# Optimization experiments

Measured on AMD Instinct MI355X. Metric: run time of the kernel, lower is better.

## Reference

```python
import jax, jax.numpy as jnp
import numpy as np

B, L, D = 4, 2048, 1024
E, F, H = 6, 1536, 512  # experts, d_ff, router hidden
TOP_K = 2
LN_EPS = 1e-5

def setup_inputs() -> dict:
    key = jax.random.key(0)
    ks = jax.random.split(key, 8)
    s = lambda fan: 1.0 / np.sqrt(fan)
    return {
        "x": jax.random.normal(ks[0], (B, L, D), jnp.float32),
        "r1_w": jax.random.normal(ks[1], (D, H), jnp.float32) * s(D),
        "r1_b": jnp.zeros((H,), jnp.float32),
        "ln_g": jnp.ones((H,), jnp.float32),
        "ln_b": jnp.zeros((H,), jnp.float32),
        "r2_w": jax.random.normal(ks[2], (H, E), jnp.float32) * s(H),
        "r2_b": jnp.zeros((E,), jnp.float32),
        "temp": jnp.ones((1,), jnp.float32),
        "route_bias": jnp.zeros((E,), jnp.float32),
        "W1": jax.random.normal(ks[3], (E, D, F), jnp.float32) * s(D),
        "b1": jnp.zeros((E, F), jnp.float32),
        "W2": jax.random.normal(ks[4], (E, F, D), jnp.float32) * s(F),
        "b2": jnp.zeros((E, D), jnp.float32),
    }

def reference(x, r1_w, r1_b, ln_g, ln_b, r2_w, r2_b, temp, route_bias, W1, b1, W2, b2):
    b, l, d = x.shape
    xf = x.reshape(-1, d)                       # [N, D]
    n = xf.shape[0]
    # Router: Linear -> LayerNorm -> GELU(exact) -> Linear
    h = xf @ r1_w + r1_b                        # [N, H]
    mu = jnp.mean(h, axis=-1, keepdims=True)
    var = jnp.mean((h - mu) ** 2, axis=-1, keepdims=True)
    h = (h - mu) * jax.lax.rsqrt(var + LN_EPS) * ln_g + ln_b
    h = jax.nn.gelu(h, approximate=False)
    logits = (h @ r2_w + r2_b) / temp + route_bias   # [N, E]
    p = jax.nn.softmax(logits, axis=-1)
    top_v, top_i = jax.lax.top_k(p, TOP_K)      # [N, k]
    probs = jnp.zeros_like(p).at[jnp.arange(n)[:, None], top_i].set(top_v)  # [N, E]
    # Dense all-expert MLPs (faithful to source, which computes every expert)
    hh = jnp.einsum('nd,edf->enf', xf, W1) + b1[:, None, :]   # [E, N, F]
    even = (jnp.arange(W1.shape[0]) % 2 == 0)[:, None, None]
    act = jnp.where(even, jax.nn.gelu(hh, approximate=False), jax.nn.silu(hh))
    eo = jnp.einsum('enf,efd->end', act, W2) + b2[:, None, :]  # [E, N, D]
    out = jnp.einsum('ne,end->nd', probs, eo)   # weighted combine
    return out.reshape(b, l, d)
```

## Files before the change

kernel.cpp:

```cpp
#include <hip/hip_runtime.h>
#include <hip/hip_bf16.h>
#include <stdint.h>

typedef __bf16 bf16;
typedef bf16 bf16x8 __attribute__((ext_vector_type(8)));
typedef bf16 bf16x4 __attribute__((ext_vector_type(4)));
typedef float f32x4 __attribute__((ext_vector_type(4)));
typedef int i32x4 __attribute__((ext_vector_type(4)));

#define N_TOK 8192
#define D_MODEL 1024
#define H_R 512
#define N_EXP 6
#define F_FF 1536
#define FLAG_CAP 1024

__device__ __forceinline__ float erf_fast(float x) {
    float ax = fabsf(x);
    float t = 1.0f / (1.0f + 0.3275911f * ax);
    float p = t * (0.254829592f + t * (-0.284496736f + t * (1.421413741f +
              t * (-1.453152027f + t * 1.061405429f))));
    float r = 1.0f - p * __expf(-ax * ax);
    return copysignf(r, x);
}
__device__ __forceinline__ float gelu_f(float x) {
    return 0.5f * x * (1.0f + erf_fast(x * 0.70710678118654752f));
}
__device__ __forceinline__ float silu_f(float x) {
    return x * (1.0f / (1.0f + __expf(-x)));
}

typedef __attribute__((address_space(1))) const void* gas1;
typedef __attribute__((address_space(3))) void* las3;

__device__ __forceinline__ void gload16(const void* g, void* l) {
    __builtin_amdgcn_global_load_lds((gas1)g, (las3)l, 16, 0, 0);
}

__device__ __forceinline__ int swz_src_q(int c) {
    return (((c & 3) - ((c >> 2) >> 1)) & 3);
}


__global__ __launch_bounds__(256) void convert_x_split(
    const float* __restrict__ x, bf16* __restrict__ xh, bf16* __restrict__ xl) {
    size_t i = ((size_t)blockIdx.x * 256 + threadIdx.x) * 8;
    f32x4 a = *(const f32x4*)(x + i);
    f32x4 b = *(const f32x4*)(x + i + 4);
    float v[8] = {a[0], a[1], a[2], a[3], b[0], b[1], b[2], b[3]};
    bf16x8 vh, vl;
    #pragma unroll
    for (int k = 0; k < 8; ++k) {
        bf16 h = (bf16)v[k];
        vh[k] = h;
        vl[k] = (bf16)(v[k] - (float)h);
    }
    *(bf16x8*)(xh + i) = vh;
    *(bf16x8*)(xl + i) = vl;
}

__global__ __launch_bounds__(256) void transpose_bf16_64(
    const float* __restrict__ in, bf16* __restrict__ out, int R, int C) {
    __shared__ float tile[64][65];
    const float* inp = in + (size_t)blockIdx.z * R * C;
    bf16* op = out + (size_t)blockIdx.z * R * C;
    int tx = threadIdx.x & 15, ty = threadIdx.x >> 4;
    int r0 = blockIdx.y * 64, c0 = blockIdx.x * 64;
    #pragma unroll
    for (int p = 0; p < 4; ++p) {
        int row = p * 16 + ty;
        f32x4 v = *(const f32x4*)(inp + (size_t)(r0 + row) * C + c0 + tx * 4);
        tile[row][tx * 4 + 0] = v[0];
        tile[row][tx * 4 + 1] = v[1];
        tile[row][tx * 4 + 2] = v[2];
        tile[row][tx * 4 + 3] = v[3];
    }
    __syncthreads();
    #pragma unroll
    for (int p = 0; p < 4; ++p) {
        int cc = p * 16 + ty;
        bf16x4 o;
        #pragma unroll
        for (int k = 0; k < 4; ++k) o[k] = (bf16)tile[tx * 4 + k][cc];
        *(bf16x4*)(op + (size_t)(c0 + cc) * R + r0 + tx * 4) = o;
    }
}

__global__ __launch_bounds__(256) void transpose_split(
    const float* __restrict__ in, bf16* __restrict__ oh, bf16* __restrict__ ol,
    int R, int C) {
    __shared__ float tile[32][33];
    int tx = threadIdx.x & 31, ty = threadIdx.x >> 5;
    int r0 = blockIdx.y * 32, c0 = blockIdx.x * 32;
    #pragma unroll
    for (int yy = ty; yy < 32; yy += 8)
        tile[yy][tx] = in[(size_t)(r0 + yy) * C + c0 + tx];
    __syncthreads();
    #pragma unroll
    for (int yy = ty; yy < 32; yy += 8) {
        float v = tile[tx][yy];
        bf16 h = (bf16)v;
        size_t o = (size_t)(c0 + yy) * R + r0 + tx;
        oh[o] = h;
        ol[o] = (bf16)(v - (float)h);
    }
}


struct SMemStd {
    alignas(16) bf16 As[128 * 32];
    alignas(16) bf16 Bs[128 * 32];
};

__device__ __forceinline__ void gemm_core_async(
    const bf16* gA0, const bf16* gA1, const bf16* gB0, const bf16* gB1,
    int K, bf16* As, bf16* Bs, f32x4 acc[4][4]) {
    const int tid = threadIdx.x;
    const int lane = tid & 63;
    const int w = tid >> 6;
    const int wm = w & 1, wn = w >> 1;
    const int lc = lane & 15;
    const int koff = ((((lane >> 4) + (lc >> 1)) & 3) * 8);
    bf16* lA0 = As + w * 512;
    bf16* lA1 = As + 2048 + w * 512;
    bf16* lB0 = Bs + w * 512;
    bf16* lB1 = Bs + 2048 + w * 512;
    for (int kb = 0; kb < K; kb += 32) {
        __syncthreads();
        gload16(gA0 + kb, lA0);
        gload16(gA1 + kb, lA1);
        gload16(gB0 + kb, lB0);
        gload16(gB1 + kb, lB1);
        __syncthreads();
        bf16x8 af[4], bfr[4];
        #pragma unroll
        for (int i = 0; i < 4; ++i)
            af[i] = *(const bf16x8*)(As + (wm * 64 + i * 16 + lc) * 32 + koff);
        #pragma unroll
        for (int j = 0; j < 4; ++j)
            bfr[j] = *(const bf16x8*)(Bs + (wn * 64 + j * 16 + lc) * 32 + koff);
        #pragma unroll
        for (int i = 0; i < 4; ++i)
            #pragma unroll
            for (int j = 0; j < 4; ++j)
                acc[i][j] = __builtin_amdgcn_mfma_f32_16x16x32_bf16(af[i], bfr[j], acc[i][j], 0, 0, 0);
    }
}


__global__ __launch_bounds__(256) void router_gemm1_3(
    const bf16* __restrict__ xh, const bf16* __restrict__ xl,
    const bf16* __restrict__ wTh, const bf16* __restrict__ wTl,
    float* __restrict__ hp0, float* __restrict__ hp1, float* __restrict__ hp2) {
    __shared__ SMemStd sm;
    const int z = blockIdx.z;
    const bf16* Ab = (z == 2) ? xl : xh;
    const bf16* Bb = (z == 1) ? wTl : wTh;
    float* hp = (z == 0) ? hp0 : (z == 1 ? hp1 : hp2);
    const int tid = threadIdx.x;
    const int mbase = blockIdx.y * 128, nbase = blockIdx.x * 128;
    int c0 = tid, c1 = tid + 256;
    const bf16* gA0 = Ab + (size_t)(mbase + (c0 >> 2)) * D_MODEL + swz_src_q(c0) * 8;
    const bf16* gA1 = Ab + (size_t)(mbase + (c1 >> 2)) * D_MODEL + swz_src_q(c1) * 8;
    const bf16* Bt = Bb + (size_t)nbase * D_MODEL;
    const bf16* gB0 = Bt + (size_t)(c0 >> 2) * D_MODEL + swz_src_q(c0) * 8;
    const bf16* gB1 = Bt + (size_t)(c1 >> 2) * D_MODEL + swz_src_q(c1) * 8;
    f32x4 acc[4][4] = {};
    gemm_core_async(gA0, gA1, gB0, gB1, D_MODEL, sm.As, sm.Bs, acc);
    const int lane = tid & 63;
    const int w = tid >> 6;
    const int wm = w & 1, wn = w >> 1;
    const int lc = lane & 15, quad = lane >> 4;
    #pragma unroll
    for (int i = 0; i < 4; ++i)
        #pragma unroll
        for (int j = 0; j < 4; ++j) {
            int col = nbase + wn * 64 + j * 16 + lc;
            #pragma unroll
            for (int r = 0; r < 4; ++r) {
                int row = mbase + wm * 64 + i * 16 + quad * 4 + r;
                hp[(size_t)row * H_R + col] = acc[i][j][r];
            }
        }
}


__global__ __launch_bounds__(256) void ln_router2(
    const float* __restrict__ hp0, const float* __restrict__ hp1,
    const float* __restrict__ hp2, const float* __restrict__ r1b,
    const float* __restrict__ g, const float* __restrict__ bta,
    const float* __restrict__ r2w, const float* __restrict__ r2b,
    const float* __restrict__ temp, const float* __restrict__ rbias,
    int* __restrict__ top_i, float* __restrict__ top_p,
    int* __restrict__ flaglist, int* __restrict__ meta) {
    __shared__ float Wl[H_R * N_EXP];
    int tid = threadIdx.x;
    for (int i = tid; i < H_R * N_EXP; i += 256) Wl[i] = r2w[i];
    __syncthreads();
    int w = tid >> 6, lane = tid & 63;
    int t = blockIdx.x * 4 + w;
    size_t rbase = (size_t)t * H_R;
    int k0 = lane * 8;
    float v[8];
    {
        f32x4 a0 = *(const f32x4*)(hp0 + rbase + k0);
        f32x4 a1 = *(const f32x4*)(hp0 + rbase + k0 + 4);
        f32x4 b0 = *(const f32x4*)(hp1 + rbase + k0);
        f32x4 b1 = *(const f32x4*)(hp1 + rbase + k0 + 4);
        f32x4 c0 = *(const f32x4*)(hp2 + rbase + k0);
        f32x4 c1 = *(const f32x4*)(hp2 + rbase + k0 + 4);
        f32x4 d0 = *(const f32x4*)(r1b + k0);
        f32x4 d1 = *(const f32x4*)(r1b + k0 + 4);
        #pragma unroll
        for (int k = 0; k < 4; ++k) {
            v[k]     = a0[k] + b0[k] + c0[k] + d0[k];
            v[k + 4] = a1[k] + b1[k] + c1[k] + d1[k];
        }
    }
    float s = 0.f;
    #pragma unroll
    for (int k = 0; k < 8; ++k) s += v[k];
    #pragma unroll
    for (int off = 32; off; off >>= 1) s += __shfl_xor(s, off);
    float mu = s * (1.0f / H_R);
    float q = 0.f;
    #pragma unroll
    for (int k = 0; k < 8; ++k) { float d = v[k] - mu; q += d * d; }
    #pragma unroll
    for (int off = 32; off; off >>= 1) q += __shfl_xor(q, off);
    float scl = 1.0f / sqrtf(q * (1.0f / H_R) + 1e-5f);
    f32x4 g0 = *(const f32x4*)(g + k0), g1 = *(const f32x4*)(g + k0 + 4);
    f32x4 b0 = *(const f32x4*)(bta + k0), b1v = *(const f32x4*)(bta + k0 + 4);
    float G[8] = {g0[0], g0[1], g0[2], g0[3], g1[0], g1[1], g1[2], g1[3]};
    float B[8] = {b0[0], b0[1], b0[2], b0[3], b1v[0], b1v[1], b1v[2], b1v[3]};
    float acc[N_EXP] = {};
    #pragma unroll
    for (int k = 0; k < 8; ++k) {
        float y = gelu_f((v[k] - mu) * scl * G[k] + B[k]);
        const float* wr = &Wl[(k0 + k) * N_EXP];
        #pragma unroll
        for (int e = 0; e < N_EXP; ++e) acc[e] += y * wr[e];
    }
    #pragma unroll
    for (int e = 0; e < N_EXP; ++e)
        #pragma unroll
        for (int off = 32; off; off >>= 1) acc[e] += __shfl_xor(acc[e], off);
    if (lane == 0) {
        float tinv = 1.0f / temp[0];
        float lg[N_EXP];
// ... 128 lines not shown
        #pragma unroll
        for (int e = 0; e < N_EXP; ++e) S[e][tid] += tmp[e];
        __syncthreads();
    }
    if (tid == 0) {
        int o = 0;
        #pragma unroll
        for (int e = 0; e < N_EXP; ++e) {
            segbase[e] = o;
            int tot = S[e][RP_T - 1];
            meta[e] = tot;
            meta[8 + e] = o;
            o += tot;
        }
        segbase[N_EXP] = o;
    }
    __syncthreads();
    int pos[N_EXP];
    #pragma unroll
    for (int e = 0; e < N_EXP; ++e)
        pos[e] = segbase[e] + S[e][tid] - cnt[e];
    #pragma unroll
    for (int k = 0; k < 2 * RP_TOK; ++k) {
        int e = e_loc[k];
        int a = 0;
        #pragma unroll
        for (int ee = 0; ee < N_EXP; ++ee) if (e == ee) a = pos[ee]++;
        atok[a] = t0 + (k >> 1);
        ainv[2 * t0 + k] = a;
    }
}


__global__ __launch_bounds__(256) void expert_gemm1(
    const bf16* __restrict__ xb, const bf16* __restrict__ W1T,
    const float* __restrict__ b1, const int* __restrict__ meta,
    const int* __restrict__ atok, bf16* __restrict__ act) {
    int e = blockIdx.z;
    int rows = meta[e];
    int mloc = blockIdx.y * 128;
    if (mloc >= rows) return;
    int base = meta[8 + e];
    __shared__ SMemStd sm;
    int tid = threadIdx.x;
    int nbase = blockIdx.x * 128;
    int c0 = tid, c1 = tid + 256;
    int r0 = mloc + (c0 >> 2); if (r0 > rows - 1) r0 = rows - 1;
    int r1 = mloc + (c1 >> 2); if (r1 > rows - 1) r1 = rows - 1;
    const bf16* gA0 = xb + (size_t)atok[base + r0] * D_MODEL + swz_src_q(c0) * 8;
    const bf16* gA1 = xb + (size_t)atok[base + r1] * D_MODEL + swz_src_q(c1) * 8;
    const bf16* Bt = W1T + ((size_t)e * F_FF + nbase) * D_MODEL;
    const bf16* gB0 = Bt + (size_t)(c0 >> 2) * D_MODEL + swz_src_q(c0) * 8;
    const bf16* gB1 = Bt + (size_t)(c1 >> 2) * D_MODEL + swz_src_q(c1) * 8;
    f32x4 acc[4][4] = {};
    gemm_core_async(gA0, gA1, gB0, gB1, D_MODEL, sm.As, sm.Bs, acc);
    const int lane = tid & 63;
    const int w = tid >> 6;
    const int wm = w & 1, wn = w >> 1;
    const int lc = lane & 15, quad = lane >> 4;
    bool odd = (e & 1) != 0;
    #pragma unroll
    for (int i = 0; i < 4; ++i)
        #pragma unroll
        for (int j = 0; j < 4; ++j) {
            int col = nbase + wn * 64 + j * 16 + lc;
            float bias = b1[e * F_FF + col];
            #pragma unroll
            for (int r = 0; r < 4; ++r) {
                int rloc = mloc + wm * 64 + i * 16 + quad * 4 + r;
                if (rloc < rows) {
                    float vv = acc[i][j][r] + bias;
                    vv = odd ? silu_f(vv) : gelu_f(vv);
                    act[(size_t)(base + rloc) * F_FF + col] = (bf16)vv;
                }
            }
        }
}

__global__ __launch_bounds__(256) void expert_gemm2(
    const bf16* __restrict__ act, const bf16* __restrict__ W2T,
    const float* __restrict__ b2, const int* __restrict__ meta,
    float* __restrict__ eo) {
    int e = blockIdx.z;
    int rows = meta[e];
    int mloc = blockIdx.y * 128;
    if (mloc >= rows) return;
    int base = meta[8 + e];
    __shared__ SMemStd sm;
    int tid = threadIdx.x;
    int nbase = blockIdx.x * 128;
    int c0 = tid, c1 = tid + 256;
    int r0 = mloc + (c0 >> 2); if (r0 > rows - 1) r0 = rows - 1;
    int r1 = mloc + (c1 >> 2); if (r1 > rows - 1) r1 = rows - 1;
    const bf16* gA0 = act + (size_t)(base + r0) * F_FF + swz_src_q(c0) * 8;
    const bf16* gA1 = act + (size_t)(base + r1) * F_FF + swz_src_q(c1) * 8;
    const bf16* Bt = W2T + ((size_t)e * D_MODEL + nbase) * F_FF;
    const bf16* gB0 = Bt + (size_t)(c0 >> 2) * F_FF + swz_src_q(c0) * 8;
    const bf16* gB1 = Bt + (size_t)(c1 >> 2) * F_FF + swz_src_q(c1) * 8;
    f32x4 acc[4][4] = {};
    gemm_core_async(gA0, gA1, gB0, gB1, F_FF, sm.As, sm.Bs, acc);
    const int lane = tid & 63;
    const int w = tid >> 6;
    const int wm = w & 1, wn = w >> 1;
    const int lc = lane & 15, quad = lane >> 4;
    #pragma unroll
    for (int i = 0; i < 4; ++i)
        #pragma unroll
        for (int j = 0; j < 4; ++j) {
            int col = nbase + wn * 64 + j * 16 + lc;
            float bias = b2[e * D_MODEL + col];
            #pragma unroll
            for (int r = 0; r < 4; ++r) {
                int rloc = mloc + wm * 64 + i * 16 + quad * 4 + r;
                if (rloc < rows)
                    eo[(size_t)(base + rloc) * D_MODEL + col] = acc[i][j][r] + bias;
            }
        }
}


__global__ __launch_bounds__(256) void combine_kernel(
    const float* __restrict__ eo, const int* __restrict__ ainv,
    const float* __restrict__ top_p, float* __restrict__ out) {
    int t = blockIdx.x;
    int s0 = ainv[2 * t], s1 = ainv[2 * t + 1];
    float p0 = top_p[2 * t], p1 = top_p[2 * t + 1];
    int c = threadIdx.x * 4;
    f32x4 a = *(const f32x4*)(eo + (size_t)s0 * D_MODEL + c);
    f32x4 b = *(const f32x4*)(eo + (size_t)s1 * D_MODEL + c);
    f32x4 o;
    #pragma unroll
    for (int k = 0; k < 4; ++k) o[k] = a[k] * p0 + b[k] * p1;
    *(f32x4*)(out + (size_t)t * D_MODEL + c) = o;
}


extern "C" void kernel_launch(void* const* d_in, const int* in_sizes, int n_in,
                              void* d_out, int out_size, void* d_ws, size_t ws_size,
                              hipStream_t stream) {
    const float* x     = (const float*)d_in[0];
    const float* r1w   = (const float*)d_in[1];
    const float* r1b   = (const float*)d_in[2];
    const float* lng   = (const float*)d_in[3];
    const float* lnb   = (const float*)d_in[4];
    const float* r2w   = (const float*)d_in[5];
    const float* r2b   = (const float*)d_in[6];
    const float* temp  = (const float*)d_in[7];
    const float* rbias = (const float*)d_in[8];
    const float* W1    = (const float*)d_in[9];
    const float* b1    = (const float*)d_in[10];
    const float* W2    = (const float*)d_in[11];
    const float* b2    = (const float*)d_in[12];
    float* out = (float*)d_out;

    char* ws = (char*)d_ws;
    size_t off = 0;
    auto alloc = [&](size_t bytes) -> void* {
        void* p = ws + off;
        off = (off + bytes + 255) & ~(size_t)255;
        return p;
    };
    bf16*  xh    = (bf16*)alloc((size_t)N_TOK * D_MODEL * 2);
    bf16*  xl    = (bf16*)alloc((size_t)N_TOK * D_MODEL * 2);
    bf16*  r1wTh = (bf16*)alloc((size_t)H_R * D_MODEL * 2);
    bf16*  r1wTl = (bf16*)alloc((size_t)H_R * D_MODEL * 2);
    bf16*  W1T   = (bf16*)alloc((size_t)N_EXP * F_FF * D_MODEL * 2);
    bf16*  W2T   = (bf16*)alloc((size_t)N_EXP * D_MODEL * F_FF * 2);
    float* hp0   = (float*)alloc((size_t)N_TOK * H_R * 4);
    int*   top_i = (int*)alloc((size_t)N_TOK * 2 * 4);
    float* top_p = (float*)alloc((size_t)N_TOK * 2 * 4);
    int*   meta  = (int*)alloc(256);
    int*   flags = (int*)alloc(FLAG_CAP * 4);
    int*   atok  = (int*)alloc((size_t)2 * N_TOK * 4);
    int*   ainv  = (int*)alloc((size_t)2 * N_TOK * 4);
    bf16*  actb  = (bf16*)alloc((size_t)2 * N_TOK * F_FF * 2);
    float* eo    = (float*)alloc((size_t)2 * N_TOK * D_MODEL * 4);
    float* hp1 = (float*)actb;
    float* hp2 = (float*)((char*)actb + (size_t)N_TOK * H_R * 4);
    (void)ws_size; (void)n_in; (void)in_sizes;

    hipMemsetAsync(meta, 0, 256, stream);

    convert_x_split<<<(N_TOK * D_MODEL) / (256 * 8), 256, 0, stream>>>(x, xh, xl);
    transpose_split<<<dim3(H_R / 32, D_MODEL / 32, 1), 256, 0, stream>>>(
        r1w, r1wTh, r1wTl, D_MODEL, H_R);
    transpose_bf16_64<<<dim3(F_FF / 64, D_MODEL / 64, N_EXP), 256, 0, stream>>>(
        W1, W1T, D_MODEL, F_FF);
    transpose_bf16_64<<<dim3(D_MODEL / 64, F_FF / 64, N_EXP), 256, 0, stream>>>(
        W2, W2T, F_FF, D_MODEL);

    router_gemm1_3<<<dim3(H_R / 128, N_TOK / 128, 3), 256, 0, stream>>>(
        xh, xl, r1wTh, r1wTl, hp0, hp1, hp2);
    ln_router2<<<N_TOK / 4, 256, 0, stream>>>(
        hp0, hp1, hp2, r1b, lng, lnb, r2w, r2b, temp, rbias, top_i, top_p, flags, meta);
    router_rescue<<<FLAG_CAP, 256, 0, stream>>>(
        x, r1w, r1b, lng, lnb, r2w, r2b, temp, rbias, flags, meta, top_i, top_p);
    route_pack<<<1, RP_T, 0, stream>>>(top_i, meta, atok, ainv);

    expert_gemm1<<<dim3(F_FF / 128, N_TOK / 128, N_EXP), 256, 0, stream>>>(
        xh, W1T, b1, meta, atok, actb);
    expert_gemm2<<<dim3(D_MODEL / 128, N_TOK / 128, N_EXP), 256, 0, stream>>>(
        actb, W2T, b2, meta, eo);
    combine_kernel<<<N_TOK, 256, 0, stream>>>(eo, ainv, top_p, out);
}
```

Baseline: 554.8 us.

## Use 256x256 double-buffered MFMA tiles with 512 threads for expert GEMMs

Adds a new GEMM core that computes 256x256 output tiles with 8 waves, a K-step of 64, a swizzled LDS layout, and double-buffered global-to-LDS loads. Each wave works through its 128x64 sub-tile in four phases, interleaving fragment loads with MFMA bursts under barriers and s_setprio. Both expert GEMMs switch to this core with 128KB of dynamic shared memory. The larger tiles raise data reuse and cut LDS traffic per FLOP. In exchange, fewer blocks are launched, there is more padded work on partial row tiles, and LDS use allows only one block per CU.

```diff
diff --git a/kernel.cpp b/kernel.cpp
--- a/kernel.cpp
+++ b/kernel.cpp
@@ -144,6 +144,131 @@
             #pragma unroll
             for (int j = 0; j < 4; ++j)
                 acc[i][j] = __builtin_amdgcn_mfma_f32_16x16x32_bf16(af[i], bfr[j], acc[i][j], 0, 0, 0);
+    }
+}
+
+
+__device__ __forceinline__ void gemm256_core(
+    const bf16* a0, const bf16* a1, const bf16* a2, const bf16* a3,
+    const bf16* b0, const bf16* b1, const bf16* b2, const bf16* b3,
+    int K, bf16* As, bf16* Bs, f32x4 acc[8][4])
+{
+    const int tid = threadIdx.x;
+    const int w = tid >> 6;
+    const int lane = tid & 63;
+    const int lc = lane & 15, qdv = lane >> 4;
+    const int wm = w & 1, wn = w >> 1;
+    const int wst = w * 512;
+    const int NT = K >> 6;
+    gload16(a0, As + wst);
+    gload16(a1, As + 4096 + wst);
+    gload16(a2, As + 8192 + wst);
+    gload16(a3, As + 12288 + wst);
+    gload16(b0, Bs + wst);
+    gload16(b1, Bs + 4096 + wst);
+    gload16(b2, Bs + 8192 + wst);
+    gload16(b3, Bs + 12288 + wst);
+    a0 += 64; a1 += 64; a2 += 64; a3 += 64;
+    b0 += 64; b1 += 64; b2 += 64; b3 += 64;
+    __syncthreads();
+    const int rA0 = wm * 128 + lc;
+    const int rB0 = wn * 64 + lc;
+    int bo = 0;
+    for (int t = 0; t < NT; ++t) {
+        const int nb = bo ^ 16384;
+        bf16x8 af[4][2], bfr[2][2];
+        if (t + 1 < NT) {
+            gload16(a0, As + nb + wst);
+            gload16(a1, As + nb + 4096 + wst);
+            gload16(a2, As + nb + 8192 + wst);
+            gload16(a3, As + nb + 12288 + wst);
+            gload16(b0, Bs + nb + wst);
+            gload16(b1, Bs + nb + 4096 + wst);
+            gload16(b2, Bs + nb + 8192 + wst);
+            gload16(b3, Bs + nb + 12288 + wst);
+            a0 += 64; a1 += 64; a2 += 64; a3 += 64;
+            b0 += 64; b1 += 64; b2 += 64; b3 += 64;
+        }
+        #pragma unroll
+        for (int i = 0; i < 4; ++i) {
+            int row = rA0 + i * 16;
+            #pragma unroll
+            for (int s = 0; s < 2; ++s)
+                af[i][s] = *(const bf16x8*)(As + bo + row * 64 + (((s * 4 + qdv) + row) & 7) * 8);
+        }
+        #pragma unroll
+        for (int j = 0; j < 2; ++j) {
+            int row = rB0 + j * 16;
+            #pragma unroll
+            for (int s = 0; s < 2; ++s)
+                bfr[j][s] = *(const bf16x8*)(Bs + bo + row * 64 + (((s * 4 + qdv) + row) & 7) * 8);
+        }
+        __builtin_amdgcn_s_barrier();
+        __builtin_amdgcn_s_setprio(1);
+        #pragma unroll
+        for (int i = 0; i < 4; ++i)
+            #pragma unroll
+            for (int j = 0; j < 2; ++j)
+                #pragma unroll
+                for (int s = 0; s < 2; ++s)
+                    acc[i][j] = __builtin_amdgcn_mfma_f32_16x16x32_bf16(af[i][s], bfr[j][s], acc[i][j], 0, 0, 0);
+        __builtin_amdgcn_s_setprio(0);
+        __builtin_amdgcn_s_barrier();
+        #pragma unroll
+        for (int j = 0; j < 2; ++j) {
+            int row = rB0 + 32 + j * 16;
+            #pragma unroll
+            for (int s = 0; s < 2; ++s)
+                bfr[j][s] = *(const bf16x8*)(Bs + bo + row * 64 + (((s * 4 + qdv) + row) & 7) * 8);
+        }
+        __builtin_amdgcn_s_barrier();
+        __builtin_amdgcn_s_setprio(1);
+        #pragma unroll
+        for (int i = 0; i < 4; ++i)
+            #pragma unroll
+            for (int j = 0; j < 2; ++j)
+                #pragma unroll
+                for (int s = 0; s < 2; ++s)
+                    acc[i][2 + j] = __builtin_amdgcn_mfma_f32_16x16x32_bf16(af[i][s], bfr[j][s], acc[i][2 + j], 0, 0, 0);
+        __builtin_amdgcn_s_setprio(0);
+        __builtin_amdgcn_s_barrier();
+        #pragma unroll
+        for (int i = 0; i < 4; ++i) {
+            int row = rA0 + 64 + i * 16;
+            #pragma unroll
+            for (int s = 0; s < 2; ++s)
+                af[i][s] = *(const bf16x8*)(As + bo + row * 64 + (((s * 4 + qdv) + row) & 7) * 8);
+        }
+        __builtin_amdgcn_s_barrier();
+        __builtin_amdgcn_s_setprio(1);
+        #pragma unroll
+        for (int i = 0; i < 4; ++i)
+            #pragma unroll
+            for (int j = 0; j < 2; ++j)
+                #pragma unroll
+                for (int s = 0; s < 2; ++s)
+                    acc[4 + i][2 + j] = __builtin_amdgcn_mfma_f32_16x16x32_bf16(af[i][s], bfr[j][s], acc[4 + i][2 + j], 0, 0, 0);
+        __builtin_amdgcn_s_setprio(0);
+        __builtin_amdgcn_s_barrier();
+        #pragma unroll
+        for (int j = 0; j < 2; ++j) {
+            int row = rB0 + j * 16;
+            #pragma unroll
+            for (int s = 0; s < 2; ++s)
+                bfr[j][s] = *(const bf16x8*)(Bs + bo + row * 64 + (((s * 4 + qdv) + row) & 7) * 8);
+        }
+        __builtin_amdgcn_s_barrier();
+        __builtin_amdgcn_s_setprio(1);
+        #pragma unroll
+        for (int i = 0; i < 4; ++i)
+            #pragma unroll
+            for (int j = 0; j < 2; ++j)
+                #pragma unroll
+                for (int s = 0; s < 2; ++s)
+                    acc[4 + i][j] = __builtin_amdgcn_mfma_f32_16x16x32_bf16(af[i][s], bfr[j][s], acc[4 + i][j], 0, 0, 0);
+        __builtin_amdgcn_s_setprio(0);
+        __syncthreads();
+        bo = nb;
     }
 }
 
@@ -409,90 +534,104 @@
 }
 
 
-__global__ __launch_bounds__(256) void expert_gemm1(
+__global__ __launch_bounds__(512, 2) void expert_gemm1(
     const bf16* __restrict__ xb, const bf16* __restrict__ W1T,
     const float* __restrict__ b1, const int* __restrict__ meta,
     const int* __restrict__ atok, bf16* __restrict__ act) {
+    extern __shared__ bf16 smem[];
     int e = blockIdx.z;
     int rows = meta[e];
-    int mloc = blockIdx.y * 128;
+    int mloc = blockIdx.y * 256;
     if (mloc >= rows) return;
     int base = meta[8 + e];
-    __shared__ SMemStd sm;
     int tid = threadIdx.x;
-    int nbase = blockIdx.x * 128;
-    int c0 = tid, c1 = tid + 256;
-    int r0 = mloc + (c0 >> 2); if (r0 > rows - 1) r0 = rows - 1;
-    int r1 = mloc + (c1 >> 2); if (r1 > rows - 1) r1 = rows - 1;
-    const bf16* gA0 = xb + (size_t)atok[base + r0] * D_MODEL + swz_src_q(c0) * 8;
-    const bf16* gA1 = xb + (size_t)atok[base + r1] * D_MODEL + swz_src_q(c1) * 8;
-    const bf16* Bt = W1T + ((size_t)e * F_FF + nbase) * D_MODEL;
-    const bf16* gB0 = Bt + (size_t)(c0 >> 2) * D_MODEL + swz_src_q(c0) * 8;
-    const bf16* gB1 = Bt + (size_t)(c1 >> 2) * D_MODEL + swz_src_q(c1) * 8;
-    f32x4 acc[4][4] = {};
-    gemm_core_async(gA0, gA1, gB0, gB1, D_MODEL, sm.As, sm.Bs, acc);
+    int nbase = blockIdx.x * 256;
+    const int sr = tid >> 3;
+    const int sc = tid & 7;
+    const bf16* ap[4];
+    const bf16* bp[4];
+    #pragma unroll
+    for (int h = 0; h < 4; ++h) {
+        int tr = h * 64 + sr;
+        int q = (sc - tr) & 7;
+        int rr = mloc + tr; if (rr > rows - 1) rr = rows - 1;
+        ap[h] = xb + (size_t)atok[base + rr] * D_MODEL + q * 8;
+        bp[h] = W1T + ((size_t)e * F_FF + nbase + tr) * D_MODEL + q * 8;
+    }
+    f32x4 acc[8][4] = {};
+    gemm256_core(ap[0], ap[1], ap[2], ap[3], bp[0], bp[1], bp[2], bp[3],
+                 D_MODEL, smem, smem + 32768, acc);
     const int lane = tid & 63;
     const int w = tid >> 6;
     const int wm = w & 1, wn = w >> 1;
-    const int lc = lane & 15, quad = lane >> 4;
-    bool odd = (e & 1) != 0;
-    #pragma unroll
-    for (int i = 0; i < 4; ++i)
-        #pragma unroll
-        for (int j = 0; j < 4; ++j) {
-            int col = nbase + wn * 64 + j * 16 + lc;
+    const int lc = lane & 15, qd = lane >> 4;
+    const bool oddE = (e & 1) != 0;
+    #pragma unroll
+    for (int ai = 0; ai < 8; ++ai) {
+        int rt = wm * 128 + (ai >> 2) * 64 + (ai & 3) * 16 + qd * 4;
+        #pragma unroll
+        for (int aj = 0; aj < 4; ++aj) {
+            int col = nbase + wn * 64 + (aj >> 1) * 32 + (aj & 1) * 16 + lc;
             float bias = b1[e * F_FF + col];
             #pragma unroll
             for (int r = 0; r < 4; ++r) {
-                int rloc = mloc + wm * 64 + i * 16 + quad * 4 + r;
+                int rloc = mloc + rt + r;
                 if (rloc < rows) {
-                    float vv = acc[i][j][r] + bias;
-                    vv = odd ? silu_f(vv) : gelu_f(vv);
+                    float vv = acc[ai][aj][r] + bias;
+                    vv = oddE ? silu_f(vv) : gelu_f(vv);
                     act[(size_t)(base + rloc) * F_FF + col] = (bf16)vv;
                 }
             }
         }
-}
-
-__global__ __launch_bounds__(256) void expert_gemm2(
+    }
+}
+
+__global__ __launch_bounds__(512, 2) void expert_gemm2(
     const bf16* __restrict__ act, const bf16* __restrict__ W2T,
     const float* __restrict__ b2, const int* __restrict__ meta,
     float* __restrict__ eo) {
+    extern __shared__ bf16 smem[];
     int e = blockIdx.z;
     int rows = meta[e];
-    int mloc = blockIdx.y * 128;
+    int mloc = blockIdx.y * 256;
     if (mloc >= rows) return;
     int base = meta[8 + e];
-    __shared__ SMemStd sm;
     int tid = threadIdx.x;
-    int nbase = blockIdx.x * 128;
-    int c0 = tid, c1 = tid + 256;
-    int r0 = mloc + (c0 >> 2); if (r0 > rows - 1) r0 = rows - 1;
-    int r1 = mloc + (c1 >> 2); if (r1 > rows - 1) r1 = rows - 1;
-    const bf16* gA0 = act + (size_t)(base + r0) * F_FF + swz_src_q(c0) * 8;
-    const bf16* gA1 = act + (size_t)(base + r1) * F_FF + swz_src_q(c1) * 8;
-    const bf16* Bt = W2T + ((size_t)e * D_MODEL + nbase) * F_FF;
-    const bf16* gB0 = Bt + (size_t)(c0 >> 2) * F_FF + swz_src_q(c0) * 8;
-    const bf16* gB1 = Bt + (size_t)(c1 >> 2) * F_FF + swz_src_q(c1) * 8;
-    f32x4 acc[4][4] = {};
-    gemm_core_async(gA0, gA1, gB0, gB1, F_FF, sm.As, sm.Bs, acc);
+    int nbase = blockIdx.x * 256;
+    const int sr = tid >> 3;
+    const int sc = tid & 7;
+    const bf16* ap[4];
+    const bf16* bp[4];
+    #pragma unroll
+    for (int h = 0; h < 4; ++h) {
+        int tr = h * 64 + sr;
+        int q = (sc - tr) & 7;
+        int rr = mloc + tr; if (rr > rows - 1) rr = rows - 1;
+        ap[h] = act + (size_t)(base + rr) * F_FF + q * 8;
+        bp[h] = W2T + ((size_t)e * D_MODEL + nbase + tr) * F_FF + q * 8;
+    }
+    f32x4 acc[8][4] = {};
+    gemm256_core(ap[0], ap[1], ap[2], ap[3], bp[0], bp[1], bp[2], bp[3],
+                 F_FF, smem, smem + 32768, acc);
     const int lane = tid & 63;
     const int w = tid >> 6;
     const int wm = w & 1, wn = w >> 1;
-    const int lc = lane & 15, quad = lane >> 4;
-    #pragma unroll
-    for (int i = 0; i < 4; ++i)
-        #pragma unroll
-        for (int j = 0; j < 4; ++j) {
-            int col = nbase + wn * 64 + j * 16 + lc;
+    const int lc = lane & 15, qd = lane >> 4;
+    #pragma unroll
+    for (int ai = 0; ai < 8; ++ai) {
+        int rt = wm * 128 + (ai >> 2) * 64 + (ai & 3) * 16 + qd * 4;
+        #pragma unroll
+        for (int aj = 0; aj < 4; ++aj) {
+            int col = nbase + wn * 64 + (aj >> 1) * 32 + (aj & 1) * 16 + lc;
             float bias = b2[e * D_MODEL + col];
             #pragma unroll
             for (int r = 0; r < 4; ++r) {
-                int rloc = mloc + wm * 64 + i * 16 + quad * 4 + r;
+                int rloc = mloc + rt + r;
                 if (rloc < rows)
-                    eo[(size_t)(base + rloc) * D_MODEL + col] = acc[i][j][r] + bias;
+                    eo[(size_t)(base + rloc) * D_MODEL + col] = acc[ai][aj][r] + bias;
             }
         }
+    }
 }
 
 
@@ -515,6 +654,14 @@
 extern "C" void kernel_launch(void* const* d_in, const int* in_sizes, int n_in,
                               void* d_out, int out_size, void* d_ws, size_t ws_size,
                               hipStream_t stream) {
+    static bool attr_done = false;
+    if (!attr_done) {
+        hipFuncSetAttribute((const void*)expert_gemm1,
+                            hipFuncAttributeMaxDynamicSharedMemorySize, 131072);
+        hipFuncSetAttribute((const void*)expert_gemm2,
+                            hipFuncAttributeMaxDynamicSharedMemorySize, 131072);
+        attr_done = true;
+    }
     const float* x     = (const float*)d_in[0];
     const float* r1w   = (const float*)d_in[1];
     const float* r1b   = (const float*)d_in[2];
@@ -574,9 +721,9 @@
         x, r1w, r1b, lng, lnb, r2w, r2b, temp, rbias, flags, meta, top_i, top_p);
     route_pack<<<1, RP_T, 0, stream>>>(top_i, meta, atok, ainv);
 
-    expert_gemm1<<<dim3(F_FF / 128, N_TOK / 128, N_EXP), 256, 0, stream>>>(
+    expert_gemm1<<<dim3(F_FF / 256, N_TOK / 256, N_EXP), 512, 131072, stream>>>(
         xh, W1T, b1, meta, atok, actb);
-    expert_gemm2<<<dim3(D_MODEL / 128, N_TOK / 128, N_EXP), 256, 0, stream>>>(
+    expert_gemm2<<<dim3(D_MODEL / 256, N_TOK / 256, N_EXP), 512, 131072, stream>>>(
         actb, W2T, b2, meta, eo);
     combine_kernel<<<N_TOK, 256, 0, stream>>>(eo, ainv, top_p, out);
 }
```

New measurement: 566.2 us. 2.1% more time.

## Double-buffer expert GEMM K-loop with BK=64 and swizzled LDS layout

Applied to the files above, without the earlier changes.

Replaces the single-buffered BK=32 async GEMM core used by both expert GEMMs with a new core that double-buffers LDS, prefetching the next 64-wide K tile while the current one feeds MFMAs. It uses a per-row XOR-style swizzle on 8-element chunks to avoid LDS bank conflicts, halves the number of barriers per K, and raises wave priority around the MFMA block. The aim is to hide global-load latency and cut synchronisation overhead. The cost is 64KB of LDS per block, which may lower occupancy.

```diff
diff --git a/kernel.cpp b/kernel.cpp
--- a/kernel.cpp
+++ b/kernel.cpp
@@ -40,6 +40,8 @@
 __device__ __forceinline__ int swz_src_q(int c) {
     return (((c & 3) - ((c >> 2) >> 1)) & 3);
 }
+
+#define GATE(N) asm volatile("s_waitcnt vmcnt(" #N ")\n\ts_barrier" ::: "memory")
 
 
 __global__ __launch_bounds__(256) void convert_x_split(
@@ -144,6 +146,77 @@
             #pragma unroll
             for (int j = 0; j < 4; ++j)
                 acc[i][j] = __builtin_amdgcn_mfma_f32_16x16x32_bf16(af[i], bfr[j], acc[i][j], 0, 0, 0);
+    }
+}
+
+
+__device__ __forceinline__ void gemm128_core(
+    const bf16* ap0, const bf16* ap1, const bf16* ap2, const bf16* ap3,
+    const bf16* bp0, const bf16* bp1, const bf16* bp2, const bf16* bp3,
+    int K, bf16* As, bf16* Bs, f32x4 acc[4][4])
+{
+    const int tid = threadIdx.x;
+    const int w = tid >> 6;
+    const int lane = tid & 63;
+    const int lc = lane & 15, qdv = lane >> 4;
+    const int wm = w & 1, wn = w >> 1;
+    const int wst = w * 512;
+    const int NT = K >> 6;
+    gload16(ap0, As + wst);
+    gload16(ap1, As + 2048 + wst);
+    gload16(ap2, As + 4096 + wst);
+    gload16(ap3, As + 6144 + wst);
+    gload16(bp0, Bs + wst);
+    gload16(bp1, Bs + 2048 + wst);
+    gload16(bp2, Bs + 4096 + wst);
+    gload16(bp3, Bs + 6144 + wst);
+    ap0 += 64; ap1 += 64; ap2 += 64; ap3 += 64;
+    bp0 += 64; bp1 += 64; bp2 += 64; bp3 += 64;
+    GATE(0);
+    const int rA0 = wm * 64 + lc;
+    const int rB0 = wn * 64 + lc;
+    int bo = 0;
+    for (int t = 0; t < NT; ++t) {
+        const int nb = bo ^ 16384;
+        const bool pref = (t + 1 < NT);
+        if (pref) {
+            gload16(ap0, As + nb + wst);
+            gload16(ap1, As + nb + 2048 + wst);
+            gload16(ap2, As + nb + 4096 + wst);
+            gload16(ap3, As + nb + 6144 + wst);
+            gload16(bp0, Bs + nb + wst);
+            gload16(bp1, Bs + nb + 2048 + wst);
+            gload16(bp2, Bs + nb + 4096 + wst);
+            gload16(bp3, Bs + nb + 6144 + wst);
+            ap0 += 64; ap1 += 64; ap2 += 64; ap3 += 64;
+            bp0 += 64; bp1 += 64; bp2 += 64; bp3 += 64;
+        }
+        bf16x8 af[4][2], bfr[4][2];
+        #pragma unroll
+        for (int i = 0; i < 4; ++i) {
+            int row = rA0 + i * 16;
+            #pragma unroll
+            for (int s = 0; s < 2; ++s)
+                af[i][s] = *(const bf16x8*)(As + bo + row * 64 + (((s * 4 + qdv) + row) & 7) * 8);
+        }
+        #pragma unroll
+        for (int j = 0; j < 4; ++j) {
+            int row = rB0 + j * 16;
+            #pragma unroll
+            for (int s = 0; s < 2; ++s)
+                bfr[j][s] = *(const bf16x8*)(Bs + bo + row * 64 + (((s * 4 + qdv) + row) & 7) * 8);
+        }
+        __builtin_amdgcn_s_setprio(1);
+        #pragma unroll
+        for (int i = 0; i < 4; ++i)
+            #pragma unroll
+            for (int j = 0; j < 4; ++j)
+                #pragma unroll
+                for (int s = 0; s < 2; ++s)
+                    acc[i][j] = __builtin_amdgcn_mfma_f32_16x16x32_bf16(af[i][s], bfr[j][s], acc[i][j], 0, 0, 0);
+        __builtin_amdgcn_s_setprio(0);
+        if (pref) GATE(0);
+        bo = nb;
     }
 }
 
@@ -413,86 +486,98 @@
     const bf16* __restrict__ xb, const bf16* __restrict__ W1T,
     const float* __restrict__ b1, const int* __restrict__ meta,
     const int* __restrict__ atok, bf16* __restrict__ act) {
+    __shared__ bf16 smem[32768];
     int e = blockIdx.z;
     int rows = meta[e];
     int mloc = blockIdx.y * 128;
     if (mloc >= rows) return;
     int base = meta[8 + e];
-    __shared__ SMemStd sm;
     int tid = threadIdx.x;
     int nbase = blockIdx.x * 128;
-    int c0 = tid, c1 = tid + 256;
-    int r0 = mloc + (c0 >> 2); if (r0 > rows - 1) r0 = rows - 1;
-    int r1 = mloc + (c1 >> 2); if (r1 > rows - 1) r1 = rows - 1;
-    const bf16* gA0 = xb + (size_t)atok[base + r0] * D_MODEL + swz_src_q(c0) * 8;
-    const bf16* gA1 = xb + (size_t)atok[base + r1] * D_MODEL + swz_src_q(c1) * 8;
-    const bf16* Bt = W1T + ((size_t)e * F_FF + nbase) * D_MODEL;
-    const bf16* gB0 = Bt + (size_t)(c0 >> 2) * D_MODEL + swz_src_q(c0) * 8;
-    const bf16* gB1 = Bt + (size_t)(c1 >> 2) * D_MODEL + swz_src_q(c1) * 8;
+    const int sr = tid >> 3;
+    const int sc = tid & 7;
+    const bf16* ap[4];
+    const bf16* bp[4];
+    #pragma unroll
+    for (int h = 0; h < 4; ++h) {
+        int tr = h * 32 + sr;
+        int q = (sc - tr) & 7;
+        int rr = mloc + tr; if (rr > rows - 1) rr = rows - 1;
+        ap[h] = xb + (size_t)atok[base + rr] * D_MODEL + q * 8;
+        bp[h] = W1T + ((size_t)e * F_FF + nbase + tr) * D_MODEL + q * 8;
+    }
     f32x4 acc[4][4] = {};
-    gemm_core_async(gA0, gA1, gB0, gB1, D_MODEL, sm.As, sm.Bs, acc);
+    gemm128_core(ap[0], ap[1], ap[2], ap[3], bp[0], bp[1], bp[2], bp[3],
+                 D_MODEL, smem, smem + 8192, acc);
     const int lane = tid & 63;
     const int w = tid >> 6;
     const int wm = w & 1, wn = w >> 1;
-    const int lc = lane & 15, quad = lane >> 4;
-    bool odd = (e & 1) != 0;
-    #pragma unroll
-    for (int i = 0; i < 4; ++i)
+    const int lc = lane & 15, qd = lane >> 4;
+    const bool oddE = (e & 1) != 0;
+    #pragma unroll
+    for (int i = 0; i < 4; ++i) {
         #pragma unroll
         for (int j = 0; j < 4; ++j) {
             int col = nbase + wn * 64 + j * 16 + lc;
             float bias = b1[e * F_FF + col];
             #pragma unroll
             for (int r = 0; r < 4; ++r) {
-                int rloc = mloc + wm * 64 + i * 16 + quad * 4 + r;
+                int rloc = mloc + wm * 64 + i * 16 + qd * 4 + r;
                 if (rloc < rows) {
                     float vv = acc[i][j][r] + bias;
-                    vv = odd ? silu_f(vv) : gelu_f(vv);
+                    vv = oddE ? silu_f(vv) : gelu_f(vv);
                     act[(size_t)(base + rloc) * F_FF + col] = (bf16)vv;
                 }
             }
         }
+    }
 }
 
 __global__ __launch_bounds__(256) void expert_gemm2(
     const bf16* __restrict__ act, const bf16* __restrict__ W2T,
     const float* __restrict__ b2, const int* __restrict__ meta,
     float* __restrict__ eo) {
+    __shared__ bf16 smem[32768];
     int e = blockIdx.z;
     int rows = meta[e];
     int mloc = blockIdx.y * 128;
     if (mloc >= rows) return;
     int base = meta[8 + e];
-    __shared__ SMemStd sm;
     int tid = threadIdx.x;
     int nbase = blockIdx.x * 128;
-    int c0 = tid, c1 = tid + 256;
-    int r0 = mloc + (c0 >> 2); if (r0 > rows - 1) r0 = rows - 1;
-    int r1 = mloc + (c1 >> 2); if (r1 > rows - 1) r1 = rows - 1;
-    const bf16* gA0 = act + (size_t)(base + r0) * F_FF + swz_src_q(c0) * 8;
-    const bf16* gA1 = act + (size_t)(base + r1) * F_FF + swz_src_q(c1) * 8;
-    const bf16* Bt = W2T + ((size_t)e * D_MODEL + nbase) * F_FF;
-    const bf16* gB0 = Bt + (size_t)(c0 >> 2) * F_FF + swz_src_q(c0) * 8;
-    const bf16* gB1 = Bt + (size_t)(c1 >> 2) * F_FF + swz_src_q(c1) * 8;
+    const int sr = tid >> 3;
+    const int sc = tid & 7;
+    const bf16* ap[4];
+    const bf16* bp[4];
+    #pragma unroll
+    for (int h = 0; h < 4; ++h) {
+        int tr = h * 32 + sr;
+        int q = (sc - tr) & 7;
+        int rr = mloc + tr; if (rr > rows - 1) rr = rows - 1;
+        ap[h] = act + (size_t)(base + rr) * F_FF + q * 8;
+        bp[h] = W2T + ((size_t)e * D_MODEL + nbase + tr) * F_FF + q * 8;
+    }
     f32x4 acc[4][4] = {};
-    gemm_core_async(gA0, gA1, gB0, gB1, F_FF, sm.As, sm.Bs, acc);
+    gemm128_core(ap[0], ap[1], ap[2], ap[3], bp[0], bp[1], bp[2], bp[3],
+                 F_FF, smem, smem + 8192, acc);
     const int lane = tid & 63;
     const int w = tid >> 6;
     const int wm = w & 1, wn = w >> 1;
-    const int lc = lane & 15, quad = lane >> 4;
-    #pragma unroll
-    for (int i = 0; i < 4; ++i)
+    const int lc = lane & 15, qd = lane >> 4;
+    #pragma unroll
+    for (int i = 0; i < 4; ++i) {
         #pragma unroll
         for (int j = 0; j < 4; ++j) {
             int col = nbase + wn * 64 + j * 16 + lc;
             float bias = b2[e * D_MODEL + col];
             #pragma unroll
             for (int r = 0; r < 4; ++r) {
-                int rloc = mloc + wm * 64 + i * 16 + quad * 4 + r;
+                int rloc = mloc + wm * 64 + i * 16 + qd * 4 + r;
                 if (rloc < rows)
                     eo[(size_t)(base + rloc) * D_MODEL + col] = acc[i][j][r] + bias;
             }
         }
+    }
 }
 
 
```

New measurement: 566.4 us. 2.1% more time.

## Double-buffer GEMM LDS loads and fuse three-pass router GEMM

Applied to the files above, without the earlier changes.

Replaces the single-buffered GEMM core with a double-buffered LDS pipeline. The next K-tile's async global-to-LDS loads are issued before the current tile's MFMAs and gated with s_waitcnt plus a barrier, and MFMA issue priority is raised. The three separate split-bf16 router GEMM passes become one kernel that runs the hi*hi, hi*lo and lo*hi products in the same loop into a single accumulator. This removes two partial-sum buffers and the extra reads in the LayerNorm kernel. Occupancy hints are added to the expert GEMMs and the weight transposes move after routing, at the cost of more LDS per block.

```diff
diff --git a/kernel.cpp b/kernel.cpp
--- a/kernel.cpp
+++ b/kernel.cpp
@@ -41,6 +41,8 @@
     return (((c & 3) - ((c >> 2) >> 1)) & 3);
 }
 
+#define GATE(N) asm volatile("s_waitcnt vmcnt(" #N ")\n\ts_barrier" ::: "memory")
+
 
 __global__ __launch_bounds__(256) void convert_x_split(
     const float* __restrict__ x, bf16* __restrict__ xh, bf16* __restrict__ xl) {
@@ -107,70 +109,127 @@
 }
 
 
-struct SMemStd {
-    alignas(16) bf16 As[128 * 32];
-    alignas(16) bf16 Bs[128 * 32];
-};
-
-__device__ __forceinline__ void gemm_core_async(
+__device__ __forceinline__ void gemm128_core(
     const bf16* gA0, const bf16* gA1, const bf16* gB0, const bf16* gB1,
-    int K, bf16* As, bf16* Bs, f32x4 acc[4][4]) {
+    int K, bf16* sm, f32x4 acc[4][4])
+{
     const int tid = threadIdx.x;
     const int lane = tid & 63;
     const int w = tid >> 6;
     const int wm = w & 1, wn = w >> 1;
     const int lc = lane & 15;
     const int koff = ((((lane >> 4) + (lc >> 1)) & 3) * 8);
-    bf16* lA0 = As + w * 512;
-    bf16* lA1 = As + 2048 + w * 512;
-    bf16* lB0 = Bs + w * 512;
-    bf16* lB1 = Bs + 2048 + w * 512;
-    for (int kb = 0; kb < K; kb += 32) {
-        __syncthreads();
-        gload16(gA0 + kb, lA0);
-        gload16(gA1 + kb, lA1);
-        gload16(gB0 + kb, lB0);
-        gload16(gB1 + kb, lB1);
-        __syncthreads();
+    gload16(gA0, sm + w * 512);
+    gload16(gA1, sm + 2048 + w * 512);
+    gload16(gB0, sm + 4096 + w * 512);
+    gload16(gB1, sm + 6144 + w * 512);
+    int bo = 0;
+    const int NT = K >> 5;
+    for (int t = 0; t < NT; ++t) {
+        const int nb = bo ^ 8192;
+        if (t + 1 < NT) {
+            const int kb = (t + 1) << 5;
+            gload16(gA0 + kb, sm + nb + w * 512);
+            gload16(gA1 + kb, sm + nb + 2048 + w * 512);
+            gload16(gB0 + kb, sm + nb + 4096 + w * 512);
+            gload16(gB1 + kb, sm + nb + 6144 + w * 512);
+            GATE(4);
+        } else {
+            GATE(0);
+        }
         bf16x8 af[4], bfr[4];
         #pragma unroll
         for (int i = 0; i < 4; ++i)
-            af[i] = *(const bf16x8*)(As + (wm * 64 + i * 16 + lc) * 32 + koff);
+            af[i] = *(const bf16x8*)(sm + bo + (wm * 64 + i * 16 + lc) * 32 + koff);
         #pragma unroll
         for (int j = 0; j < 4; ++j)
-            bfr[j] = *(const bf16x8*)(Bs + (wn * 64 + j * 16 + lc) * 32 + koff);
+            bfr[j] = *(const bf16x8*)(sm + bo + 4096 + (wn * 64 + j * 16 + lc) * 32 + koff);
+        __builtin_amdgcn_s_barrier();
+        __builtin_amdgcn_s_setprio(1);
         #pragma unroll
         for (int i = 0; i < 4; ++i)
             #pragma unroll
             for (int j = 0; j < 4; ++j)
                 acc[i][j] = __builtin_amdgcn_mfma_f32_16x16x32_bf16(af[i], bfr[j], acc[i][j], 0, 0, 0);
-    }
-}
-
-
-__global__ __launch_bounds__(256) void router_gemm1_3(
+        __builtin_amdgcn_s_setprio(0);
+        bo = nb;
+    }
+}
+
+
+__global__ __launch_bounds__(256, 2) void router_gemm_fused(
     const bf16* __restrict__ xh, const bf16* __restrict__ xl,
     const bf16* __restrict__ wTh, const bf16* __restrict__ wTl,
-    float* __restrict__ hp0, float* __restrict__ hp1, float* __restrict__ hp2) {
-    __shared__ SMemStd sm;
-    const int z = blockIdx.z;
-    const bf16* Ab = (z == 2) ? xl : xh;
-    const bf16* Bb = (z == 1) ? wTl : wTh;
-    float* hp = (z == 0) ? hp0 : (z == 1 ? hp1 : hp2);
+    float* __restrict__ hp) {
+    __shared__ bf16 smem[32768];
     const int tid = threadIdx.x;
     const int mbase = blockIdx.y * 128, nbase = blockIdx.x * 128;
-    int c0 = tid, c1 = tid + 256;
-    const bf16* gA0 = Ab + (size_t)(mbase + (c0 >> 2)) * D_MODEL + swz_src_q(c0) * 8;
-    const bf16* gA1 = Ab + (size_t)(mbase + (c1 >> 2)) * D_MODEL + swz_src_q(c1) * 8;
-    const bf16* Bt = Bb + (size_t)nbase * D_MODEL;
-    const bf16* gB0 = Bt + (size_t)(c0 >> 2) * D_MODEL + swz_src_q(c0) * 8;
-    const bf16* gB1 = Bt + (size_t)(c1 >> 2) * D_MODEL + swz_src_q(c1) * 8;
+    const int c0 = tid, c1 = tid + 256;
+    const size_t ra0 = (size_t)(mbase + (c0 >> 2)) * D_MODEL + swz_src_q(c0) * 8;
+    const size_t ra1 = (size_t)(mbase + (c1 >> 2)) * D_MODEL + swz_src_q(c1) * 8;
+    const size_t rb0 = (size_t)(nbase + (c0 >> 2)) * D_MODEL + swz_src_q(c0) * 8;
+    const size_t rb1 = (size_t)(nbase + (c1 >> 2)) * D_MODEL + swz_src_q(c1) * 8;
+    const bf16 *pxh0 = xh + ra0, *pxh1 = xh + ra1;
+    const bf16 *pxl0 = xl + ra0, *pxl1 = xl + ra1;
+    const bf16 *pwh0 = wTh + rb0, *pwh1 = wTh + rb1;
+    const bf16 *pwl0 = wTl + rb0, *pwl1 = wTl + rb1;
+    const int w = tid >> 6, lane = tid & 63;
+    const int wm = w & 1, wn = w >> 1, lc = lane & 15;
+    const int koff = ((((lane >> 4) + (lc >> 1)) & 3) * 8);
+    const int ws = w * 512;
     f32x4 acc[4][4] = {};
-    gemm_core_async(gA0, gA1, gB0, gB1, D_MODEL, sm.As, sm.Bs, acc);
-    const int lane = tid & 63;
-    const int w = tid >> 6;
-    const int wm = w & 1, wn = w >> 1;
-    const int lc = lane & 15, quad = lane >> 4;
+    gload16(pxh0, smem + ws);
+    gload16(pxh1, smem + 2048 + ws);
+    gload16(pxl0, smem + 4096 + ws);
+    gload16(pxl1, smem + 6144 + ws);
+    gload16(pwh0, smem + 8192 + ws);
+    gload16(pwh1, smem + 10240 + ws);
+    gload16(pwl0, smem + 12288 + ws);
+    gload16(pwl1, smem + 14336 + ws);
+    int bo = 0;
+    for (int t = 0; t < D_MODEL / 32; ++t) {
+        const int nb = bo ^ 16384;
+        if (t + 1 < D_MODEL / 32) {
+            const int kb = (t + 1) << 5;
+            gload16(pxh0 + kb, smem + nb + ws);
+            gload16(pxh1 + kb, smem + nb + 2048 + ws);
+            gload16(pxl0 + kb, smem + nb + 4096 + ws);
+            gload16(pxl1 + kb, smem + nb + 6144 + ws);
+            gload16(pwh0 + kb, smem + nb + 8192 + ws);
+            gload16(pwh1 + kb, smem + nb + 10240 + ws);
+            gload16(pwl0 + kb, smem + nb + 12288 + ws);
+            gload16(pwl1 + kb, smem + nb + 14336 + ws);
+            GATE(8);
+        } else {
+            GATE(0);
+        }
+        bf16x8 ah[4], al[4], bh[4], bl[4];
+        #pragma unroll
+        for (int i = 0; i < 4; ++i) {
+            const int ro = (wm * 64 + i * 16 + lc) * 32 + koff;
+            ah[i] = *(const bf16x8*)(smem + bo + ro);
+            al[i] = *(const bf16x8*)(smem + bo + 4096 + ro);
+        }
+        #pragma unroll
+        for (int j = 0; j < 4; ++j) {
+            const int ro = (wn * 64 + j * 16 + lc) * 32 + koff;
+            bh[j] = *(const bf16x8*)(smem + bo + 8192 + ro);
+            bl[j] = *(const bf16x8*)(smem + bo + 12288 + ro);
+        }
+        __builtin_amdgcn_s_barrier();
+        __builtin_amdgcn_s_setprio(1);
+        #pragma unroll
+        for (int i = 0; i < 4; ++i)
+            #pragma unroll
+            for (int j = 0; j < 4; ++j) {
+                acc[i][j] = __builtin_amdgcn_mfma_f32_16x16x32_bf16(ah[i], bh[j], acc[i][j], 0, 0, 0);
+                acc[i][j] = __builtin_amdgcn_mfma_f32_16x16x32_bf16(ah[i], bl[j], acc[i][j], 0, 0, 0);
+                acc[i][j] = __builtin_amdgcn_mfma_f32_16x16x32_bf16(al[i], bh[j], acc[i][j], 0, 0, 0);
+            }
+        __builtin_amdgcn_s_setprio(0);
+        bo = nb;
+    }
+    const int quad = lane >> 4;
     #pragma unroll
     for (int i = 0; i < 4; ++i)
         #pragma unroll
@@ -186,8 +245,7 @@
 
 
 __global__ __launch_bounds__(256) void ln_router2(
-    const float* __restrict__ hp0, const float* __restrict__ hp1,
-    const float* __restrict__ hp2, const float* __restrict__ r1b,
+    const float* __restrict__ hp, const float* __restrict__ r1b,
     const float* __restrict__ g, const float* __restrict__ bta,
     const float* __restrict__ r2w, const float* __restrict__ r2b,
     const float* __restrict__ temp, const float* __restrict__ rbias,
@@ -203,18 +261,14 @@
     int k0 = lane * 8;
     float v[8];
     {
-        f32x4 a0 = *(const f32x4*)(hp0 + rbase + k0);
-        f32x4 a1 = *(const f32x4*)(hp0 + rbase + k0 + 4);
-        f32x4 b0 = *(const f32x4*)(hp1 + rbase + k0);
-        f32x4 b1 = *(const f32x4*)(hp1 + rbase + k0 + 4);
-        f32x4 c0 = *(const f32x4*)(hp2 + rbase + k0);
-        f32x4 c1 = *(const f32x4*)(hp2 + rbase + k0 + 4);
+        f32x4 a0 = *(const f32x4*)(hp + rbase + k0);
+        f32x4 a1 = *(const f32x4*)(hp + rbase + k0 + 4);
         f32x4 d0 = *(const f32x4*)(r1b + k0);
         f32x4 d1 = *(const f32x4*)(r1b + k0 + 4);
         #pragma unroll
         for (int k = 0; k < 4; ++k) {
-            v[k]     = a0[k] + b0[k] + c0[k] + d0[k];
-            v[k + 4] = a1[k] + b1[k] + c1[k] + d1[k];
+            v[k]     = a0[k] + d0[k];
+            v[k + 4] = a1[k] + d1[k];
         }
     }
     float s = 0.f;
@@ -409,16 +463,16 @@
 }
 
 
-__global__ __launch_bounds__(256) void expert_gemm1(
+__global__ __launch_bounds__(256, 4) void expert_gemm1(
     const bf16* __restrict__ xb, const bf16* __restrict__ W1T,
     const float* __restrict__ b1, const int* __restrict__ meta,
     const int* __restrict__ atok, bf16* __restrict__ act) {
+    __shared__ bf16 smem[16384];
     int e = blockIdx.z;
     int rows = meta[e];
     int mloc = blockIdx.y * 128;
     if (mloc >= rows) return;
     int base = meta[8 + e];
-    __shared__ SMemStd sm;
     int tid = threadIdx.x;
     int nbase = blockIdx.x * 128;
     int c0 = tid, c1 = tid + 256;
@@ -430,40 +484,41 @@
     const bf16* gB0 = Bt + (size_t)(c0 >> 2) * D_MODEL + swz_src_q(c0) * 8;
     const bf16* gB1 = Bt + (size_t)(c1 >> 2) * D_MODEL + swz_src_q(c1) * 8;
     f32x4 acc[4][4] = {};
-    gemm_core_async(gA0, gA1, gB0, gB1, D_MODEL, sm.As, sm.Bs, acc);
+    gemm128_core(gA0, gA1, gB0, gB1, D_MODEL, smem, acc);
     const int lane = tid & 63;
     const int w = tid >> 6;
     const int wm = w & 1, wn = w >> 1;
-    const int lc = lane & 15, quad = lane >> 4;
-    bool odd = (e & 1) != 0;
-    #pragma unroll
-    for (int i = 0; i < 4; ++i)
+    const int lc = lane & 15, qd = lane >> 4;
+    const bool oddE = (e & 1) != 0;
+    #pragma unroll
+    for (int i = 0; i < 4; ++i) {
         #pragma unroll
         for (int j = 0; j < 4; ++j) {
             int col = nbase + wn * 64 + j * 16 + lc;
             float bias = b1[e * F_FF + col];
             #pragma unroll
             for (int r = 0; r < 4; ++r) {
-                int rloc = mloc + wm * 64 + i * 16 + quad * 4 + r;
+                int rloc = mloc + wm * 64 + i * 16 + qd * 4 + r;
                 if (rloc < rows) {
                     float vv = acc[i][j][r] + bias;
-                    vv = odd ? silu_f(vv) : gelu_f(vv);
+                    vv = oddE ? silu_f(vv) : gelu_f(vv);
                     act[(size_t)(base + rloc) * F_FF + col] = (bf16)vv;
                 }
             }
         }
-}
-
-__global__ __launch_bounds__(256) void expert_gemm2(
+    }
+}
+
+__global__ __launch_bounds__(256, 4) void expert_gemm2(
     const bf16* __restrict__ act, const bf16* __restrict__ W2T,
     const float* __restrict__ b2, const int* __restrict__ meta,
     float* __restrict__ eo) {
+    __shared__ bf16 smem[16384];
     int e = blockIdx.z;
     int rows = meta[e];
     int mloc = blockIdx.y * 128;
     if (mloc >= rows) return;
     int base = meta[8 + e];
-    __shared__ SMemStd sm;
     int tid = threadIdx.x;
     int nbase = blockIdx.x * 128;
     int c0 = tid, c1 = tid + 256;
@@ -475,24 +530,25 @@
     const bf16* gB0 = Bt + (size_t)(c0 >> 2) * F_FF + swz_src_q(c0) * 8;
     const bf16* gB1 = Bt + (size_t)(c1 >> 2) * F_FF + swz_src_q(c1) * 8;
     f32x4 acc[4][4] = {};
-    gemm_core_async(gA0, gA1, gB0, gB1, F_FF, sm.As, sm.Bs, acc);
+    gemm128_core(gA0, gA1, gB0, gB1, F_FF, smem, acc);
     const int lane = tid & 63;
     const int w = tid >> 6;
     const int wm = w & 1, wn = w >> 1;
-    const int lc = lane & 15, quad = lane >> 4;
-    #pragma unroll
-    for (int i = 0; i < 4; ++i)
+    const int lc = lane & 15, qd = lane >> 4;
+    #pragma unroll
+    for (int i = 0; i < 4; ++i) {
         #pragma unroll
         for (int j = 0; j < 4; ++j) {
             int col = nbase + wn * 64 + j * 16 + lc;
             float bias = b2[e * D_MODEL + col];
             #pragma unroll
             for (int r = 0; r < 4; ++r) {
-                int rloc = mloc + wm * 64 + i * 16 + quad * 4 + r;
+                int rloc = mloc + wm * 64 + i * 16 + qd * 4 + r;
                 if (rloc < rows)
                     eo[(size_t)(base + rloc) * D_MODEL + col] = acc[i][j][r] + bias;
             }
         }
+    }
 }
 
 
@@ -543,7 +599,7 @@
     bf16*  r1wTl = (bf16*)alloc((size_t)H_R * D_MODEL * 2);
     bf16*  W1T   = (bf16*)alloc((size_t)N_EXP * F_FF * D_MODEL * 2);
     bf16*  W2T   = (bf16*)alloc((size_t)N_EXP * D_MODEL * F_FF * 2);
-    float* hp0   = (float*)alloc((size_t)N_TOK * H_R * 4);
+    float* hp    = (float*)alloc((size_t)N_TOK * H_R * 4);
     int*   top_i = (int*)alloc((size_t)N_TOK * 2 * 4);
     float* top_p = (float*)alloc((size_t)N_TOK * 2 * 4);
     int*   meta  = (int*)alloc(256);
@@ -552,8 +608,6 @@
     int*   ainv  = (int*)alloc((size_t)2 * N_TOK * 4);
     bf16*  actb  = (bf16*)alloc((size_t)2 * N_TOK * F_FF * 2);
     float* eo    = (float*)alloc((size_t)2 * N_TOK * D_MODEL * 4);
-    float* hp1 = (float*)actb;
-    float* hp2 = (float*)((char*)actb + (size_t)N_TOK * H_R * 4);
     (void)ws_size; (void)n_in; (void)in_sizes;
 
     hipMemsetAsync(meta, 0, 256, stream);
@@ -561,18 +615,19 @@
     convert_x_split<<<(N_TOK * D_MODEL) / (256 * 8), 256, 0, stream>>>(x, xh, xl);
     transpose_split<<<dim3(H_R / 32, D_MODEL / 32, 1), 256, 0, stream>>>(
         r1w, r1wTh, r1wTl, D_MODEL, H_R);
+
+    router_gemm_fused<<<dim3(H_R / 128, N_TOK / 128, 1), 256, 0, stream>>>(
+        xh, xl, r1wTh, r1wTl, hp);
+    ln_router2<<<N_TOK / 4, 256, 0, stream>>>(
+        hp, r1b, lng, lnb, r2w, r2b, temp, rbias, top_i, top_p, flags, meta);
+    router_rescue<<<FLAG_CAP, 256, 0, stream>>>(
+        x, r1w, r1b, lng, lnb, r2w, r2b, temp, rbias, flags, meta, top_i, top_p);
+    route_pack<<<1, RP_T, 0, stream>>>(top_i, meta, atok, ainv);
+
     transpose_bf16_64<<<dim3(F_FF / 64, D_MODEL / 64, N_EXP), 256, 0, stream>>>(
         W1, W1T, D_MODEL, F_FF);
     transpose_bf16_64<<<dim3(D_MODEL / 64, F_FF / 64, N_EXP), 256, 0, stream>>>(
         W2, W2T, F_FF, D_MODEL);
-
-    router_gemm1_3<<<dim3(H_R / 128, N_TOK / 128, 3), 256, 0, stream>>>(
-        xh, xl, r1wTh, r1wTl, hp0, hp1, hp2);
-    ln_router2<<<N_TOK / 4, 256, 0, stream>>>(
-        hp0, hp1, hp2, r1b, lng, lnb, r2w, r2b, temp, rbias, top_i, top_p, flags, meta);
-    router_rescue<<<FLAG_CAP, 256, 0, stream>>>(
-        x, r1w, r1b, lng, lnb, r2w, r2b, temp, rbias, flags, meta, top_i, top_p);
-    route_pack<<<1, RP_T, 0, stream>>>(top_i, meta, atok, ainv);
 
     expert_gemm1<<<dim3(F_FF / 128, N_TOK / 128, N_EXP), 256, 0, stream>>>(
         xh, W1T, b1, meta, atok, actb);
```

Result: faster. 537.4 us (-3.1%).
